# Performance work log

Measured on AMD Instinct MI355X. Metric: run time of the kernel, lower is better.

## Reference

```python
import jax, jax.numpy as jnp
import numpy as np

N_NODES = 100000
N_EDGES = 3200000
NFEAT, NHID, NCLASS = 512, 256, 64


def spmm(rows, cols, vals, x):
    # out[i] = sum_{e: rows[e]==i} vals[e] * x[cols[e]]
    msgs = vals[:, None] * x[cols]  # [E, F]
    return jax.ops.segment_sum(msgs, rows, num_segments=N_NODES)


def setup_inputs() -> dict:
    key = jax.random.key(0)
    ks = jax.random.split(key, 12)
    x = jax.random.normal(ks[0], (N_NODES, NFEAT), dtype=jnp.float32)
    adj_rows = jax.random.randint(ks[1], (N_EDGES,), 0, N_NODES, dtype=jnp.int32)
    adj_cols = jax.random.randint(ks[2], (N_EDGES,), 0, N_NODES, dtype=jnp.int32)
    adj_vals = jax.random.uniform(ks[3], (N_EDGES,), dtype=jnp.float32)
    # xavier-uniform style init for linear weights
    def xavier(k, fan_in, fan_out):
        a = np.sqrt(6.0 / (fan_in + fan_out)).astype(np.float32)
        return jax.random.uniform(k, (fan_in, fan_out), minval=-a, maxval=a, dtype=jnp.float32)
    W1 = xavier(ks[4], NFEAT, NHID)
    b1 = jnp.zeros((NHID,), dtype=jnp.float32)
    W2 = xavier(ks[5], NHID, NCLASS)
    b2 = jnp.zeros((NCLASS,), dtype=jnp.float32)
    Wres = xavier(ks[6], NHID, NCLASS)
    bres = jnp.zeros((NCLASS,), dtype=jnp.float32)
    return {"x": x, "adj_rows": adj_rows, "adj_cols": adj_cols, "adj_vals": adj_vals,
            "W1": W1, "b1": b1, "W2": W2, "b2": b2, "Wres": Wres, "bres": bres}


def reference(x, adj_rows, adj_cols, adj_vals, W1, b1, W2, b2, Wres, bres):
    # layer 1: spmm -> linear (res_con True but last_hidden is None -> no residual)
    h = spmm(adj_rows, adj_cols, adj_vals, x)          # [N, NFEAT]
    h = h @ W1 + b1                                    # [N, NHID]
    last_hidden = h
    # dropout in eval mode: identity
    # layer 2: spmm -> linear -> relu + res(last_hidden) since NHID != NCLASS
    o = spmm(adj_rows, adj_cols, adj_vals, h)          # [N, NHID]
    o = o @ W2 + b2                                    # [N, NCLASS]
    o = jax.nn.relu(o) + (last_hidden @ Wres + bres)   # [N, NCLASS]
    return o
```

## Files before the change

### kernel.cpp

```cpp
#include <hip/hip_runtime.h>

#define N_NODES 100000
#define N_EDGES 3200000
#define NFEAT 512
#define NHID 256
#define NCLASS 64
#define FCAT 128

#define RPB 32
#define NB 3125
#define CHUNK 32768
#define NCH 98

#define ISC20 (1.0f / 1048576.0f)
#define ISC14 (1.0f / 16384.0f)
#define ISC10 (1.0f / 1024.0f)

typedef __attribute__((ext_vector_type(8))) short short8;
typedef __attribute__((ext_vector_type(4))) float f32x4;

static __device__ __forceinline__ unsigned short f2bf(float f) {
    unsigned u = __float_as_uint(f);
    unsigned r = (u + 0x7FFF + ((u >> 16) & 1)) >> 16;
    return (unsigned short)r;
}
static __device__ __forceinline__ short8 cvt8(float4 x, float4 y) {
    short8 r;
    r[0] = (short)f2bf(x.x); r[1] = (short)f2bf(x.y);
    r[2] = (short)f2bf(x.z); r[3] = (short)f2bf(x.w);
    r[4] = (short)f2bf(y.x); r[5] = (short)f2bf(y.y);
    r[6] = (short)f2bf(y.z); r[7] = (short)f2bf(y.w);
    return r;
}
__device__ __forceinline__ void gload_lds16(const unsigned short* g, unsigned short* l) {
    __builtin_amdgcn_global_load_lds(
        (const __attribute__((address_space(1))) unsigned int*)g,
        (__attribute__((address_space(3))) unsigned int*)l, 16, 0, 0);
}
static __device__ __forceinline__ int f2q10(float a) {
    return __float2int_rn(fminf(fmaxf(a, -15.98f), 15.98f) * 1024.f);
}

__global__ __launch_bounds__(256) void k_fusedA(const float* __restrict__ W1,
                                                const float* __restrict__ W2,
                                                const float* __restrict__ Wres,
                                                const float* __restrict__ b1,
                                                const float* __restrict__ bres,
                                                unsigned short* __restrict__ WT,
                                                float* __restrict__ c2,
                                                float* __restrict__ cr,
                                                const int* __restrict__ rows,
                                                int* __restrict__ HT) {
    __shared__ int h[NB];
    int tid = threadIdx.x;
    if (blockIdx.x < 256) {
        int k = blockIdx.x * 2 + (tid >> 7);
        int j = tid & 127;
        const float* wb = (j < NCLASS) ? W2 : Wres;
        int jj = j & (NCLASS - 1);
        const float* w1row = W1 + (size_t)k * NHID;
        float acc = 0.f;
        for (int m = 0; m < NHID; ++m)
            acc += w1row[m] * wb[(size_t)m * NCLASS + jj];
        WT[(size_t)j * NFEAT + k] = f2bf(acc);
        return;
    }
    if (blockIdx.x == 256) {
        if (tid < 128) {
            int j = tid;
            const float* wb = (j < NCLASS) ? W2 : Wres;
            int jj = j & (NCLASS - 1);
            float acc = 0.f;
            for (int m = 0; m < NHID; ++m)
                acc += b1[m] * wb[(size_t)m * NCLASS + jj];
            if (j < NCLASS) c2[jj] = acc;
            else            cr[jj] = acc + bres[jj];
        }
        return;
    }
    int c = blockIdx.x - 257;
    for (int i = tid; i < NB; i += 256) h[i] = 0;
    __syncthreads();
    int e0 = c * CHUNK;
    int eend = e0 + CHUNK; if (eend > N_EDGES) eend = N_EDGES;
    int i = e0 + tid;
    for (; i + 7 * 256 < eend; i += 8 * 256) {
        int r[8];
#pragma unroll
        for (int u = 0; u < 8; ++u) r[u] = rows[i + u * 256];
#pragma unroll
        for (int u = 0; u < 8; ++u) atomicAdd(&h[r[u] >> 5], 1);
    }
    for (; i < eend; i += 256)
        atomicAdd(&h[rows[i] >> 5], 1);
    __syncthreads();
    for (int k = tid; k < NB; k += 256)
        HT[(size_t)k * NCH + c] = h[k];
}

__global__ void k_scan_chunks(const int* __restrict__ HT, int* __restrict__ OFS,
                              int* __restrict__ T) {
    int b = blockIdx.x;
    int lane = threadIdx.x;
    const int* hb = HT + (size_t)b * NCH;
    int run = 0;
    for (int c0 = 0; c0 < NCH; c0 += 64) {
        int idx = c0 + lane;
        int v = (idx < NCH) ? hb[idx] : 0;
        int inc = v;
#pragma unroll
        for (int d = 1; d < 64; d <<= 1) {
            int t = __shfl_up(inc, d);
            if (lane >= d) inc += t;
        }
        if (idx < NCH) OFS[(size_t)idx * NB + b] = run + inc - v;
        run += __shfl(inc, 63);
    }
    if (lane == 0) T[b] = run;
}

__global__ void k_scan_base(const int* __restrict__ T, int* __restrict__ base) {
    int lane = threadIdx.x;
    int run = 0;
    for (int c0 = 0; c0 < NB; c0 += 64) {
        int idx = c0 + lane;
        int v = (idx < NB) ? T[idx] : 0;
        int inc = v;
#pragma unroll
        for (int d = 1; d < 64; d <<= 1) {
            int t = __shfl_up(inc, d);
            if (lane >= d) inc += t;
        }
        if (idx < NB) base[idx] = run + inc - v;
        run += __shfl(inc, 63);
    }
    if (lane == 0) base[NB] = run;
}

#define GBK 64
__global__ __launch_bounds__(256) void k_fusedB(const int* __restrict__ rows,
                                                const int* __restrict__ cols,
                                                const float* __restrict__ vals,
                                                const int* __restrict__ OFS,
                                                const int* __restrict__ base,
                                                int2* __restrict__ stage,
                                                const float* __restrict__ X,
                                                const unsigned short* __restrict__ WT,
                                                unsigned* __restrict__ A2) {
    __shared__ __align__(16) char smem[32768];
    int tid = threadIdx.x;

    if (blockIdx.x < NCH) {
        int* cur = (int*)smem;
        int c = blockIdx.x;
        for (int i = tid; i < NB; i += 256)
            cur[i] = base[i] + OFS[(size_t)c * NB + i];
        __syncthreads();
        int e0 = c * CHUNK;
        int eend = e0 + CHUNK; if (eend > N_EDGES) eend = N_EDGES;
        int i = e0 + tid;
        for (; i + 7 * 256 < eend; i += 8 * 256) {
            int r[8], cc[8]; float v[8];
#pragma unroll
            for (int u = 0; u < 8; ++u) r[u] = rows[i + u * 256];
#pragma unroll
            for (int u = 0; u < 8; ++u) cc[u] = cols[i + u * 256];
#pragma unroll
            for (int u = 0; u < 8; ++u) v[u] = vals[i + u * 256];
            int p[8];
#pragma unroll
            for (int u = 0; u < 8; ++u) p[u] = atomicAdd(&cur[r[u] >> 5], 1);
#pragma unroll
            for (int u = 0; u < 8; ++u)
                stage[p[u]] = make_int2((int)(((unsigned)(r[u] & 31) << 27) |
                                              ((unsigned)cc[u] << 8)),
                                        __float2int_rn(v[u] * 1024.f));
        }
        for (; i < eend; i += 256) {
            int r = rows[i];
            int p = atomicAdd(&cur[r >> 5], 1);
            stage[p] = make_int2((int)(((unsigned)(r & 31) << 27) | ((unsigned)cols[i] << 8)),
                                 __float2int_rn(vals[i] * 1024.f));
        }
        return;
    }

    unsigned short* Bs = (unsigned short*)smem;
    int g = blockIdx.x - NCH;
    int lane = tid & 63, w = tid >> 6;
    int lr = lane & 15, ls = lane >> 4;
    int row = g * 64 + w * 16 + lr;
    if (row >= N_NODES) row = N_NODES - 1;
    const float* pA = X + (size_t)row * NFEAT;

#define STAGE(buf, k0)                                                         \
    {                                                                          \
        _Pragma("unroll")                                                      \
        for (int q = 0; q < 4; ++q) {                                          \
            int sidx = q * 256 + tid;                                          \
            int n = sidx >> 3, c8 = sidx & 7;                                  \
            const unsigned short* src =                                        \
                WT + (size_t)n * NFEAT + (k0) + ((c8 ^ (n & 7)) << 3);         \
            unsigned short* dst =                                              \
                Bs + (size_t)(buf) * FCAT * GBK + (size_t)(q * 256 + w * 64) * 8; \
            gload_lds16(src, dst);                                             \
        }                                                                      \
    }

    f32x4 acc[8] = {};
    STAGE(0, 0);
    __syncthreads();
    int cur = 0;

#pragma unroll
    for (int t = 0; t < 8; ++t) {
        const int k0 = t * GBK;
        float4 a00 = *(const float4*)(pA + k0 + ls * 8);
        float4 a01 = *(const float4*)(pA + k0 + ls * 8 + 4);
        float4 a10 = *(const float4*)(pA + k0 + 32 + ls * 8);
        float4 a11 = *(const float4*)(pA + k0 + 32 + ls * 8 + 4);
        if (t < 7) STAGE(cur ^ 1, k0 + GBK);

        short8 af0 = cvt8(a00, a01);
        short8 af1 = cvt8(a10, a11);
        const unsigned short* bb = Bs + (size_t)cur * FCAT * GBK;
#pragma unroll
        for (int nf = 0; nf < 8; ++nf) {
            int n = nf * 16 + lr;
            int p0 = ls ^ (n & 7);
            int p1 = (4 + ls) ^ (n & 7);
            short8 b0 = *(const short8*)(bb + (size_t)n * 64 + p0 * 8);
            short8 b1 = *(const short8*)(bb + (size_t)n * 64 + p1 * 8);
            acc[nf] = __builtin_amdgcn_mfma_f32_16x16x32_bf16(af0, b0, acc[nf], 0, 0, 0);
            acc[nf] = __builtin_amdgcn_mfma_f32_16x16x32_bf16(af1, b1, acc[nf], 0, 0, 0);
        }
        __syncthreads();
        cur ^= 1;
    }
#undef STAGE

#pragma unroll
    for (int j = 0; j < 4; ++j) {
        int gr = g * 64 + w * 16 + ls * 4 + j;
        if (gr < N_NODES) {
#pragma unroll
            for (int nf = 0; nf < 4; ++nf) {
                int il = f2q10(acc[nf][j]);
                int ih = f2q10(acc[nf + 4][j]);
                A2[(size_t)gr * 64 + nf * 16 + lr] =
                    ((unsigned)il & 0xffffu) | ((unsigned)ih << 16);
            }
        }
    }
}

__global__ __launch_bounds__(256) void k_spmm1(const unsigned* __restrict__ A2,
                                               const int* __restrict__ base,
                                               const int2* __restrict__ stage,
                                               unsigned short* __restrict__ S1a,
                                               float* __restrict__ S1r) {
    __shared__ int acc[RPB][FCAT];
    int b = blockIdx.x, tid = threadIdx.x;
    int wv = tid >> 6, lane = tid & 63;
    unsigned lane4 = (unsigned)lane << 2;
    int4* az = (int4*)&acc[0][0];
    for (int i = tid; i < RPB * FCAT / 4; i += 256) az[i] = make_int4(0, 0, 0, 0);
    __syncthreads();

    const char* A2b = (const char*)A2;

    int s = base[b], e = base[b + 1];
    int per = (e - s + 3) >> 2;
    int ws = s + wv * per;
    int we = ws + per; if (we > e) we = e;
    int t = ws;
    for (; t + 16 <= we; t += 16) {
        int2 cv[16];
#pragma unroll
        for (int u = 0; u < 16; ++u) cv[u] = stage[t + u];
        unsigned p[16];
#pragma unroll
        for (int u = 0; u < 16; ++u)
            p[u] = *(const unsigned*)(A2b + ((((unsigned)cv[u].x) & 0x01FFFF00u) | lane4));
#pragma unroll
        for (int u = 0; u < 16; ++u) {
            int v10 = cv[u].y;
            int alo = (int)(short)(p[u] & 0xffffu);
            int ahi = (int)p[u] >> 16;
            int rl = (int)(((unsigned)cv[u].x) >> 27);
            atomicAdd(&acc[rl][lane],      __mul24(alo, v10));
            atomicAdd(&acc[rl][lane + 64], __mul24(ahi, v10));
        }
    }
    for (; t < we; ++t) {
        int2 cv = stage[t];
        unsigned p = *(const unsigned*)(A2b + ((((unsigned)cv.x) & 0x01FFFF00u) | lane4));
        int v10 = cv.y;
        int alo = (int)(short)(p & 0xffffu);
        int ahi = (int)p >> 16;
        int rl = (int)(((unsigned)cv.x) >> 27);
        atomicAdd(&acc[rl][lane],      __mul24(alo, v10));
        atomicAdd(&acc[rl][lane + 64], __mul24(ahi, v10));
    }
    __syncthreads();

#pragma unroll
    for (int rr = 0; rr < 8; ++rr) {
        int r = wv * 8 + rr;
        int node = b * RPB + r;
        int sf = (acc[r][lane] + 2048) >> 12;
        sf = max(-32760, min(32760, sf));
        S1a[(size_t)node * 64 + (lane & 31) * 2 + (lane >> 5)] = (unsigned short)sf;
        S1r[(size_t)node * 64 + lane] = (float)acc[r][lane + 64] * ISC20;
    }
}

__global__ __launch_bounds__(256) void k_spmm2_out(const unsigned* __restrict__ S1aP,
                                                   const float* __restrict__ S1r,
                                                   const int* __restrict__ base,
                                                   const int2* __restrict__ stage,
                                                   const float* __restrict__ c2,
                                                   const float* __restrict__ cr,
                                                   const float* __restrict__ b2,
                                                   float* __restrict__ out) {
    __shared__ int acc[RPB][NCLASS];
    __shared__ int rs[RPB];
    int b = blockIdx.x, tid = threadIdx.x;
    int wv = tid >> 6, lane = tid & 63;
    int h = lane >> 5, l5 = lane & 31;
    unsigned l54 = (unsigned)l5 << 2;
    int4* az = (int4*)&acc[0][0];
    for (int i = tid; i < RPB * NCLASS / 4; i += 256) az[i] = make_int4(0, 0, 0, 0);
    if (tid < RPB) rs[tid] = 0;
    __syncthreads();

    const char* Sb = (const char*)S1aP;

    int s = base[b], e = base[b + 1];
    int per = (e - s + 3) >> 2;
    int ws = s + wv * per;
    int we = ws + per; if (we > e) we = e;
    int t = ws;
    for (; t + 16 <= we; t += 16) {
        int2 cv[8];
#pragma unroll
        for (int u = 0; u < 8; ++u) cv[u] = stage[t + u * 2 + h];
        unsigned p[8];
#pragma unroll
        for (int u = 0; u < 8; ++u)
            p[u] = *(const unsigned*)(Sb + (((((unsigned)cv[u].x) & 0x01FFFF00u) >> 1) | l54));
#pragma unroll
        for (int u = 0; u < 8; ++u) {
            int v10 = cv[u].y;
            int slo = (int)(short)(p[u] & 0xffffu);
            int shi = (int)p[u] >> 16;
            int rl = (int)(((unsigned)cv[u].x) >> 27);
            atomicAdd(&acc[rl][l5],      (__mul24(slo, v10) + 8) >> 4);
            atomicAdd(&acc[rl][l5 + 32], (__mul24(shi, v10) + 8) >> 4);
            if (l5 == 0) atomicAdd(&rs[rl], v10);
        }
    }
    for (; t < we; t += 2) {
        int idx = t + h;
        bool act = idx < we;
        int2 cv = stage[act ? idx : t];
        unsigned p = *(const unsigned*)(Sb + (((((unsigned)cv.x) & 0x01FFFF00u) >> 1) | l54));
        int v10 = cv.y;
        int slo = (int)(short)(p & 0xffffu);
        int shi = (int)p >> 16;
        int rl = (int)(((unsigned)cv.x) >> 27);
        if (act) {
            atomicAdd(&acc[rl][l5],      (__mul24(slo, v10) + 8) >> 4);
            atomicAdd(&acc[rl][l5 + 32], (__mul24(shi, v10) + 8) >> 4);
            if (l5 == 0) atomicAdd(&rs[rl], v10);
        }
    }
    __syncthreads();

#pragma unroll
    for (int rr = 0; rr < 8; ++rr) {
        int r = wv * 8 + rr;
        int node = b * RPB + r;
        float facc = (float)acc[r][lane] * ISC14;
        float rsum = (float)rs[r] * ISC10;
        float o = facc + rsum * c2[lane] + b2[lane];
        float res = S1r[(size_t)node * 64 + lane] + cr[lane];
        out[(size_t)node * 64 + lane] = fmaxf(o, 0.f) + res;
    }
}

extern "C" void kernel_launch(void* const* d_in, const int* in_sizes, int n_in,
                              void* d_out, int out_size, void* d_ws, size_t ws_size,
                              hipStream_t stream) {
    const float* x        = (const float*)d_in[0];
    const int*   adj_rows = (const int*)d_in[1];
    const int*   adj_cols = (const int*)d_in[2];
    const float* adj_vals = (const float*)d_in[3];
    const float* W1       = (const float*)d_in[4];
    const float* b1       = (const float*)d_in[5];
    const float* W2       = (const float*)d_in[6];
    const float* b2       = (const float*)d_in[7];
    const float* Wres     = (const float*)d_in[8];
    const float* bres     = (const float*)d_in[9];
    float* out = (float*)d_out;

    char* ws = (char*)d_ws;
    size_t off = 0;
    auto alloc = [&](size_t bytes) {
        size_t o = off;
        off += (bytes + 511) & ~511ULL;
        return o;
    };

    unsigned short* WT  = (unsigned short*)(ws + alloc((size_t)NFEAT * FCAT * 2));
    float* c2           = (float*)(ws + alloc(NCLASS * 4));
    float* cr           = (float*)(ws + alloc(NCLASS * 4));
    int2* stage         = (int2*)(ws + alloc((size_t)N_EDGES * 8));
    unsigned* A2        = (unsigned*)(ws + alloc((size_t)N_NODES * 64 * 4));
    unsigned* S1a       = (unsigned*)(ws + alloc((size_t)N_NODES * 32 * 4));
    char* s1r_region    = ws + alloc((size_t)N_NODES * 64 * 4);
    float* S1r          = (float*)s1r_region;
    int*   HT           = (int*)s1r_region;
    int*   OFS          = (int*)(s1r_region + (((size_t)NB * NCH * 4 + 511) & ~511ULL));
    int*   T            = (int*)(ws + alloc((size_t)NB * 4));
    int*   base         = (int*)(ws + alloc((size_t)(NB + 1) * 4));
    (void)ws_size; (void)in_sizes; (void)n_in; (void)out_size;

    k_fusedA<<<257 + NCH, 256, 0, stream>>>(W1, W2, Wres, b1, bres, WT, c2, cr,
                                            adj_rows, HT);

    k_scan_chunks<<<NB, 64, 0, stream>>>(HT, OFS, T);
    k_scan_base<<<1, 64, 0, stream>>>(T, base);

    k_fusedB<<<NCH + (N_NODES + 63) / 64, 256, 0, stream>>>(
        adj_rows, adj_cols, adj_vals, OFS, base, stage, x, WT, A2);

    k_spmm1<<<NB, 256, 0, stream>>>(A2, base, stage, (unsigned short*)S1a, S1r);

    k_spmm2_out<<<NB, 256, 0, stream>>>(S1a, S1r, base, stage, c2, cr, b2, out);
}
```

Measured before the change: 366.8 us.

## Pack staged edges into 32-bit words and halve edge chunk size

```diff
diff --git a/kernel.cpp b/kernel.cpp
--- a/kernel.cpp
+++ b/kernel.cpp
@@ -9,8 +9,8 @@
 
 #define RPB 32
 #define NB 3125
-#define CHUNK 32768
-#define NCH 98
+#define CHUNK 16384
+#define NCH 196
 
 #define ISC20 (1.0f / 1048576.0f)
 #define ISC14 (1.0f / 16384.0f)
@@ -143,7 +143,7 @@
                                                 const float* __restrict__ vals,
                                                 const int* __restrict__ OFS,
                                                 const int* __restrict__ base,
-                                                int2* __restrict__ stage,
+                                                unsigned* __restrict__ stage,
                                                 const float* __restrict__ X,
                                                 const unsigned short* __restrict__ WT,
                                                 unsigned* __restrict__ A2) {
@@ -171,16 +171,17 @@
 #pragma unroll
             for (int u = 0; u < 8; ++u) p[u] = atomicAdd(&cur[r[u] >> 5], 1);
 #pragma unroll
-            for (int u = 0; u < 8; ++u)
-                stage[p[u]] = make_int2((int)(((unsigned)(r[u] & 31) << 27) |
-                                              ((unsigned)cc[u] << 8)),
-                                        __float2int_rn(v[u] * 1024.f));
+            for (int u = 0; u < 8; ++u) {
+                unsigned v10 = min(1023u, (unsigned)__float2int_rn(v[u] * 1024.f));
+                stage[p[u]] = (((unsigned)(r[u] & 31)) << 27) |
+                              (((unsigned)cc[u]) << 10) | v10;
+            }
         }
         for (; i < eend; i += 256) {
             int r = rows[i];
             int p = atomicAdd(&cur[r >> 5], 1);
-            stage[p] = make_int2((int)(((unsigned)(r & 31) << 27) | ((unsigned)cols[i] << 8)),
-                                 __float2int_rn(vals[i] * 1024.f));
+            unsigned v10 = min(1023u, (unsigned)__float2int_rn(vals[i] * 1024.f));
+            stage[p] = (((unsigned)(r & 31)) << 27) | (((unsigned)cols[i]) << 10) | v10;
         }
         return;
     }
@@ -256,7 +257,7 @@
 
 __global__ __launch_bounds__(256) void k_spmm1(const unsigned* __restrict__ A2,
                                                const int* __restrict__ base,
-                                               const int2* __restrict__ stage,
+                                               const unsigned* __restrict__ stage,
                                                unsigned short* __restrict__ S1a,
                                                float* __restrict__ S1r) {
     __shared__ int acc[RPB][FCAT];
@@ -275,30 +276,30 @@
     int we = ws + per; if (we > e) we = e;
     int t = ws;
     for (; t + 16 <= we; t += 16) {
-        int2 cv[16];
+        unsigned cv[16];
 #pragma unroll
         for (int u = 0; u < 16; ++u) cv[u] = stage[t + u];
         unsigned p[16];
 #pragma unroll
         for (int u = 0; u < 16; ++u)
-            p[u] = *(const unsigned*)(A2b + ((((unsigned)cv[u].x) & 0x01FFFF00u) | lane4));
+            p[u] = *(const unsigned*)(A2b + (((cv[u] & 0x07FFFC00u) >> 2) | lane4));
 #pragma unroll
         for (int u = 0; u < 16; ++u) {
-            int v10 = cv[u].y;
+            int v10 = (int)(cv[u] & 0x3FFu);
             int alo = (int)(short)(p[u] & 0xffffu);
             int ahi = (int)p[u] >> 16;
-            int rl = (int)(((unsigned)cv[u].x) >> 27);
+            int rl = (int)(cv[u] >> 27);
             atomicAdd(&acc[rl][lane],      __mul24(alo, v10));
             atomicAdd(&acc[rl][lane + 64], __mul24(ahi, v10));
         }
     }
     for (; t < we; ++t) {
-        int2 cv = stage[t];
-        unsigned p = *(const unsigned*)(A2b + ((((unsigned)cv.x) & 0x01FFFF00u) | lane4));
-        int v10 = cv.y;
+        unsigned cv = stage[t];
+        unsigned p = *(const unsigned*)(A2b + (((cv & 0x07FFFC00u) >> 2) | lane4));
+        int v10 = (int)(cv & 0x3FFu);
         int alo = (int)(short)(p & 0xffffu);
         int ahi = (int)p >> 16;
-        int rl = (int)(((unsigned)cv.x) >> 27);
+        int rl = (int)(cv >> 27);
         atomicAdd(&acc[rl][lane],      __mul24(alo, v10));
         atomicAdd(&acc[rl][lane + 64], __mul24(ahi, v10));
     }
@@ -318,7 +319,7 @@
 __global__ __launch_bounds__(256) void k_spmm2_out(const unsigned* __restrict__ S1aP,
                                                    const float* __restrict__ S1r,
                                                    const int* __restrict__ base,
-                                                   const int2* __restrict__ stage,
+                                                   const unsigned* __restrict__ stage,
                                                    const float* __restrict__ c2,
                                                    const float* __restrict__ cr,
                                                    const float* __restrict__ b2,
@@ -342,19 +343,19 @@
     int we = ws + per; if (we > e) we = e;
     int t = ws;
     for (; t + 16 <= we; t += 16) {
-        int2 cv[8];
+        unsigned cv[8];
 #pragma unroll
         for (int u = 0; u < 8; ++u) cv[u] = stage[t + u * 2 + h];
         unsigned p[8];
 #pragma unroll
         for (int u = 0; u < 8; ++u)
-            p[u] = *(const unsigned*)(Sb + (((((unsigned)cv[u].x) & 0x01FFFF00u) >> 1) | l54));
+            p[u] = *(const unsigned*)(Sb + (((cv[u] & 0x07FFFC00u) >> 3) | l54));
 #pragma unroll
         for (int u = 0; u < 8; ++u) {
-            int v10 = cv[u].y;
+            int v10 = (int)(cv[u] & 0x3FFu);
             int slo = (int)(short)(p[u] & 0xffffu);
             int shi = (int)p[u] >> 16;
-            int rl = (int)(((unsigned)cv[u].x) >> 27);
+            int rl = (int)(cv[u] >> 27);
             atomicAdd(&acc[rl][l5],      (__mul24(slo, v10) + 8) >> 4);
             atomicAdd(&acc[rl][l5 + 32], (__mul24(shi, v10) + 8) >> 4);
             if (l5 == 0) atomicAdd(&rs[rl], v10);
@@ -363,12 +364,12 @@
     for (; t < we; t += 2) {
         int idx = t + h;
         bool act = idx < we;
-        int2 cv = stage[act ? idx : t];
-        unsigned p = *(const unsigned*)(Sb + (((((unsigned)cv.x) & 0x01FFFF00u) >> 1) | l54));
-        int v10 = cv.y;
+        unsigned cv = stage[act ? idx : t];
+        unsigned p = *(const unsigned*)(Sb + (((cv & 0x07FFFC00u) >> 3) | l54));
+        int v10 = (int)(cv & 0x3FFu);
         int slo = (int)(short)(p & 0xffffu);
         int shi = (int)p >> 16;
-        int rl = (int)(((unsigned)cv.x) >> 27);
+        int rl = (int)(cv >> 27);
         if (act) {
             atomicAdd(&acc[rl][l5],      (__mul24(slo, v10) + 8) >> 4);
             atomicAdd(&acc[rl][l5 + 32], (__mul24(shi, v10) + 8) >> 4);
@@ -415,7 +416,7 @@
     unsigned short* WT  = (unsigned short*)(ws + alloc((size_t)NFEAT * FCAT * 2));
     float* c2           = (float*)(ws + alloc(NCLASS * 4));
     float* cr           = (float*)(ws + alloc(NCLASS * 4));
-    int2* stage         = (int2*)(ws + alloc((size_t)N_EDGES * 8));
+    unsigned* stage     = (unsigned*)(ws + alloc((size_t)N_EDGES * 4));
     unsigned* A2        = (unsigned*)(ws + alloc((size_t)N_NODES * 64 * 4));
     unsigned* S1a       = (unsigned*)(ws + alloc((size_t)N_NODES * 32 * 4));
     char* s1r_region    = ws + alloc((size_t)N_NODES * 64 * 4);
```

New measurement: 323.6 us. 1.13x faster.
